# Kernel optimization log

Hardware: AMD Instinct MI355X
Metric: run time of the kernel (lower is better)

## Reference

```python
import jax, jax.numpy as jnp
import numpy as np

TOP_K = 2

def setup_inputs() -> dict:
    key = jax.random.key(0)
    k1, k2 = jax.random.split(key)
    D, E = 4096, 64
    hidden_states = jax.random.normal(k1, (2, 8192, D), dtype=jnp.float32)
    W = jax.random.normal(k2, (E, D), dtype=jnp.float32) / np.sqrt(D)
    b = jnp.zeros((E,), dtype=jnp.float32)
    return {"hidden_states": hidden_states, "W": W, "b": b}

def reference(hidden_states, W, b):
    # gate: logits [B, S, E]
    logits = jnp.einsum('bsd,ed->bse', hidden_states, W) + b
    scores = jax.nn.softmax(logits, axis=-1)
    top_k_values, top_k_indices = jax.lax.top_k(scores, TOP_K)
    return ((top_k_indices, top_k_values), scores)
```

## Files before the change

kernel.cpp:

```cpp
#include <hip/hip_runtime.h>
#include <math.h>

#define D_DIM 4096
#define E_DIM 64
#define TM 32
#define CHK 128
#define NCH (D_DIM / CHK)
#define HC 16384
#define SROW 68
#define WSCALE 1024.0f
#define ISCALE (1.0f / 1024.0f)

typedef __attribute__((ext_vector_type(8))) __fp16 f16x8;
typedef __attribute__((ext_vector_type(2))) __fp16 f16x2;
typedef __attribute__((ext_vector_type(4))) float f32x4;

__device__ inline void split2(const f32x4 a0, const f32x4 a1, f16x8& fh, f16x8& fl) {
    float f[8] = {a0[0], a0[1], a0[2], a0[3], a1[0], a1[1], a1[2], a1[3]};
    union { f16x8 v; f16x2 p[4]; } H, L;
    #pragma unroll
    for (int j = 0; j < 4; ++j) {
        const f16x2 h = __builtin_amdgcn_cvt_pkrtz(f[2*j], f[2*j+1]);
        const float r0 = f[2*j]     - (float)h[0];
        const float r1 = f[2*j + 1] - (float)h[1];
        H.p[j] = h;
        L.p[j] = __builtin_amdgcn_cvt_pkrtz(r0, r1);
    }
    fh = H.v; fl = L.v;
}

__global__ __launch_bounds__(512, 4) void router_fused(
    const float* __restrict__ hs,
    const float* __restrict__ W,
    const float* __restrict__ bias,
    float* __restrict__ out,
    int nTok)
{
    __shared__ __attribute__((aligned(16))) __fp16 wbuf[2][HC];

    const int tid  = threadIdx.x;
    const int lane = tid & 63;
    const int wv   = tid >> 6;
    const int th   = wv >> 2;
    const int eq   = wv & 3;
    const int l15  = lane & 15;
    const int lq   = lane >> 4;
    const int tb   = blockIdx.x * TM;

    const float* aptr = hs + (size_t)(tb + th * 16 + l15) * D_DIM + lq * 8;
    const int erow = (eq * 16 + l15) * 128;
    const int g0   = lq ^ (l15 & 7);

    const int we = tid >> 3;
    const int wa = tid & 7;
    const float* wptr = W + (size_t)we * D_DIM + wa * 16;
    const int wbase = we * 128;
    const int gp0 = ((2 * wa)     ^ (we & 7)) * 8;
    const int gp1 = ((2 * wa + 1) ^ (we & 7)) * 8;

    f32x4 acc = (f32x4){0.f, 0.f, 0.f, 0.f};
    f32x4 ca[8], pa[8], wr[4];

    auto loadA = [&](int ch, f32x4* dst) {
        const float* p = aptr + ch * CHK;
        #pragma unroll
        for (int s = 0; s < 4; ++s) {
            dst[2*s]     = *(const f32x4*)(p + s * 32);
            dst[2*s + 1] = *(const f32x4*)(p + s * 32 + 4);
        }
    };
    auto loadW = [&](int ch) {
        const float* p = wptr + ch * CHK;
        wr[0] = *(const f32x4*)(p);
        wr[1] = *(const f32x4*)(p + 4);
        wr[2] = *(const f32x4*)(p + 8);
        wr[3] = *(const f32x4*)(p + 12);
    };
    auto storeW = [&](int buf) {
        f16x8 h0, l0, h1, l1;
        split2(wr[0] * WSCALE, wr[1] * WSCALE, h0, l0);
        split2(wr[2] * WSCALE, wr[3] * WSCALE, h1, l1);
        __fp16* b = &wbuf[buf][0];
        *(f16x8*)&b[wbase + gp0]        = h0;  *(f16x8*)&b[wbase + gp1]        = h1;
        *(f16x8*)&b[8192 + wbase + gp0] = l0;  *(f16x8*)&b[8192 + wbase + gp1] = l1;
    };
    auto compute = [&](const f32x4* a, int buf) {
        #pragma unroll
        for (int s = 0; s < 4; ++s) {
            f16x8 ah, al;
            split2(a[2*s], a[2*s + 1], ah, al);
            const int go = (g0 ^ (s << 2)) * 8;
            const f16x8 bh = *(const f16x8*)&wbuf[buf][erow + go];
            const f16x8 bl = *(const f16x8*)&wbuf[buf][8192 + erow + go];
            acc = __builtin_amdgcn_mfma_f32_16x16x32_f16(ah, bh, acc, 0, 0, 0);
            acc = __builtin_amdgcn_mfma_f32_16x16x32_f16(ah, bl, acc, 0, 0, 0);
            acc = __builtin_amdgcn_mfma_f32_16x16x32_f16(al, bh, acc, 0, 0, 0);
        }
    };

    loadA(0, ca);
    loadW(0);
    storeW(0);
    __syncthreads();
    int buf = 0;
    #pragma unroll 1
    for (int ch = 0; ch < NCH; ++ch) {
        const bool last = (ch == NCH - 1);
        if (!last) {
            loadA(ch + 1, pa);
            loadW(ch + 1);
        }
        compute(ca, buf);
        if (!last) storeW(buf ^ 1);
        __syncthreads();
        if (!last) {
            #pragma unroll
            for (int i = 0; i < 8; ++i) ca[i] = pa[i];
        }
        buf ^= 1;
    }

    float* sc_lds = (float*)&wbuf[0][0];
    {
        const int e = eq * 16 + l15;
        #pragma unroll
        for (int r = 0; r < 4; ++r)
            sc_lds[(th * 16 + lq * 4 + r) * SROW + e] = acc[r] * ISCALE;
    }
    __syncthreads();

    if (tid < TM * 4) {
        const int token = tid >> 2;
        const int g     = tid & 3;
        const int gtok  = tb + token;

        float* out_idx = out;
        float* out_val = out + (size_t)nTok * 2;
        float* sc      = out + (size_t)nTok * 4;

        const float* srcl = sc_lds + token * SROW + g * 16;
        float v[16];
        #pragma unroll
        for (int j = 0; j < 4; ++j) {
            const f32x4 x = *(const f32x4*)(srcl + j * 4);
            const f32x4 b = *(const f32x4*)(bias + g * 16 + j * 4);
            v[j*4 + 0] = x[0] + b[0];
            v[j*4 + 1] = x[1] + b[1];
            v[j*4 + 2] = x[2] + b[2];
            v[j*4 + 3] = x[3] + b[3];
        }

        float b1 = -INFINITY, b2 = -INFINITY;
        int i1 = 0, i2 = 0;
        #pragma unroll
        for (int j = 0; j < 16; ++j) {
            const float x = v[j];
            const int idx = g * 16 + j;
            if (x > b1)      { b2 = b1; i2 = i1; b1 = x; i1 = idx; }
            else if (x > b2) { b2 = x; i2 = idx; }
        }
        #pragma unroll
        for (int d = 1; d <= 2; d <<= 1) {
            const float ob1 = __shfl_xor(b1, d);
            const int   oi1 = __shfl_xor(i1, d);
            const float ob2 = __shfl_xor(b2, d);
            const int   oi2 = __shfl_xor(i2, d);
            if (ob1 > b1 || (ob1 == b1 && oi1 < i1)) {
                if (b1 > ob2 || (b1 == ob2 && i1 < oi2)) { b2 = b1; i2 = i1; }
                else                                     { b2 = ob2; i2 = oi2; }
                b1 = ob1; i1 = oi1;
            } else {
                if (ob1 > b2 || (ob1 == b2 && oi1 < i2)) { b2 = ob1; i2 = oi1; }
            }
        }
        const float m = b1;

        float e[16];
        float s = 0.f;
        #pragma unroll
        for (int j = 0; j < 16; ++j) { e[j] = __expf(v[j] - m); s += e[j]; }
        s += __shfl_xor(s, 1);
        s += __shfl_xor(s, 2);
        const float inv = 1.f / s;

        if (g == 0) {
            out_idx[(size_t)gtok * 2 + 0] = (float)i1;
            out_idx[(size_t)gtok * 2 + 1] = (float)i2;
            out_val[(size_t)gtok * 2 + 0] = inv;
            out_val[(size_t)gtok * 2 + 1] = __expf(b2 - m) * inv;
        }

        float* dstg = sc + (size_t)gtok * E_DIM + g * 16;
        #pragma unroll
        for (int j = 0; j < 4; ++j) {
            f32x4 o;
            o[0] = e[j*4 + 0] * inv;
            o[1] = e[j*4 + 1] * inv;
            o[2] = e[j*4 + 2] * inv;
            o[3] = e[j*4 + 3] * inv;
            *(f32x4*)(dstg + j * 4) = o;
        }
    }
}

extern "C" void kernel_launch(void* const* d_in, const int* in_sizes, int n_in,
                              void* d_out, int out_size, void* d_ws, size_t ws_size,
                              hipStream_t stream) {
    const float* hs = (const float*)d_in[0];
    const float* W  = (const float*)d_in[1];
    const float* b  = (const float*)d_in[2];
    float* out = (float*)d_out;
    const int nTok = in_sizes[0] / D_DIM;

    router_fused<<<dim3(nTok / TM), dim3(512), 0, stream>>>(hs, W, b, out, nTok);
}
```

Measured before the change: 443.6 us.

## Split-K across waves with W read directly from global, drop LDS weight staging

Each block now handles 16 tokens with 4 waves, each wave covering a quarter of the K dimension for all 64 experts. Partial sums are reduced through LDS before the softmax/top-k. W is loaded straight from global/L2 and split into fp16 hi/lo in registers, so the shared-memory weight double-buffer and the per-chunk __syncthreads go away. In exchange, every block re-reads and re-converts W, which multiplies W traffic and conversion ALU work, and the final reduction is small extra LDS work.

```diff
diff --git a/kernel.cpp b/kernel.cpp
--- a/kernel.cpp
+++ b/kernel.cpp
@@ -3,10 +3,10 @@
 
 #define D_DIM 4096
 #define E_DIM 64
-#define TM 32
-#define CHK 128
-#define NCH (D_DIM / CHK)
-#define HC 16384
+#define TM 16
+#define KQ 1024
+#define CHK 64
+#define NCH (KQ / CHK)
 #define SROW 68
 #define WSCALE 1024.0f
 #define ISCALE (1.0f / 1024.0f)
@@ -29,104 +29,73 @@
     fh = H.v; fl = L.v;
 }
 
-__global__ __launch_bounds__(512, 4) void router_fused(
+__global__ __launch_bounds__(256, 4) void router_fused(
     const float* __restrict__ hs,
     const float* __restrict__ W,
     const float* __restrict__ bias,
     float* __restrict__ out,
     int nTok)
 {
-    __shared__ __attribute__((aligned(16))) __fp16 wbuf[2][HC];
+    __shared__ float sc_lds[4][TM][SROW];
 
     const int tid  = threadIdx.x;
     const int lane = tid & 63;
     const int wv   = tid >> 6;
-    const int th   = wv >> 2;
-    const int eq   = wv & 3;
     const int l15  = lane & 15;
     const int lq   = lane >> 4;
     const int tb   = blockIdx.x * TM;
 
-    const float* aptr = hs + (size_t)(tb + th * 16 + l15) * D_DIM + lq * 8;
-    const int erow = (eq * 16 + l15) * 128;
-    const int g0   = lq ^ (l15 & 7);
+    const float* aptr = hs + (size_t)(tb + l15) * D_DIM + wv * KQ + lq * 8;
+    const float* wptr = W + (size_t)l15 * D_DIM + wv * KQ + lq * 8;
 
-    const int we = tid >> 3;
-    const int wa = tid & 7;
-    const float* wptr = W + (size_t)we * D_DIM + wa * 16;
-    const int wbase = we * 128;
-    const int gp0 = ((2 * wa)     ^ (we & 7)) * 8;
-    const int gp1 = ((2 * wa + 1) ^ (we & 7)) * 8;
+    f32x4 acc[4];
+    #pragma unroll
+    for (int t = 0; t < 4; ++t) acc[t] = (f32x4){0.f, 0.f, 0.f, 0.f};
 
-    f32x4 acc = (f32x4){0.f, 0.f, 0.f, 0.f};
-    f32x4 ca[8], pa[8], wr[4];
+    f32x4 ca[4], pa[4];
 
     auto loadA = [&](int ch, f32x4* dst) {
         const float* p = aptr + ch * CHK;
+        dst[0] = *(const f32x4*)(p);
+        dst[1] = *(const f32x4*)(p + 4);
+        dst[2] = *(const f32x4*)(p + 32);
+        dst[3] = *(const f32x4*)(p + 36);
+    };
+    auto computeChunk = [&](int ch, const f32x4* a) {
         #pragma unroll
-        for (int s = 0; s < 4; ++s) {
-            dst[2*s]     = *(const f32x4*)(p + s * 32);
-            dst[2*s + 1] = *(const f32x4*)(p + s * 32 + 4);
-        }
-    };
-    auto loadW = [&](int ch) {
-        const float* p = wptr + ch * CHK;
-        wr[0] = *(const f32x4*)(p);
-        wr[1] = *(const f32x4*)(p + 4);
-        wr[2] = *(const f32x4*)(p + 8);
-        wr[3] = *(const f32x4*)(p + 12);
-    };
-    auto storeW = [&](int buf) {
-        f16x8 h0, l0, h1, l1;
-        split2(wr[0] * WSCALE, wr[1] * WSCALE, h0, l0);
-        split2(wr[2] * WSCALE, wr[3] * WSCALE, h1, l1);
-        __fp16* b = &wbuf[buf][0];
-        *(f16x8*)&b[wbase + gp0]        = h0;  *(f16x8*)&b[wbase + gp1]        = h1;
-        *(f16x8*)&b[8192 + wbase + gp0] = l0;  *(f16x8*)&b[8192 + wbase + gp1] = l1;
-    };
-    auto compute = [&](const f32x4* a, int buf) {
-        #pragma unroll
-        for (int s = 0; s < 4; ++s) {
+        for (int s = 0; s < 2; ++s) {
             f16x8 ah, al;
             split2(a[2*s], a[2*s + 1], ah, al);
-            const int go = (g0 ^ (s << 2)) * 8;
-            const f16x8 bh = *(const f16x8*)&wbuf[buf][erow + go];
-            const f16x8 bl = *(const f16x8*)&wbuf[buf][8192 + erow + go];
-            acc = __builtin_amdgcn_mfma_f32_16x16x32_f16(ah, bh, acc, 0, 0, 0);
-            acc = __builtin_amdgcn_mfma_f32_16x16x32_f16(ah, bl, acc, 0, 0, 0);
-            acc = __builtin_amdgcn_mfma_f32_16x16x32_f16(al, bh, acc, 0, 0, 0);
+            #pragma unroll
+            for (int t = 0; t < 4; ++t) {
+                const float* p = wptr + (size_t)t * 16 * D_DIM + ch * CHK + s * 32;
+                const f32x4 w0 = *(const f32x4*)(p);
+                const f32x4 w1 = *(const f32x4*)(p + 4);
+                f16x8 bh, bl;
+                split2(w0 * WSCALE, w1 * WSCALE, bh, bl);
+                acc[t] = __builtin_amdgcn_mfma_f32_16x16x32_f16(ah, bh, acc[t], 0, 0, 0);
+                acc[t] = __builtin_amdgcn_mfma_f32_16x16x32_f16(ah, bl, acc[t], 0, 0, 0);
+                acc[t] = __builtin_amdgcn_mfma_f32_16x16x32_f16(al, bh, acc[t], 0, 0, 0);
+            }
         }
     };
 
     loadA(0, ca);
-    loadW(0);
-    storeW(0);
-    __syncthreads();
-    int buf = 0;
     #pragma unroll 1
     for (int ch = 0; ch < NCH; ++ch) {
-        const bool last = (ch == NCH - 1);
-        if (!last) {
-            loadA(ch + 1, pa);
-            loadW(ch + 1);
+        if (ch + 1 < NCH) loadA(ch + 1, pa);
+        computeChunk(ch, ca);
+        if (ch + 1 < NCH) {
+            #pragma unroll
+            for (int i = 0; i < 4; ++i) ca[i] = pa[i];
         }
-        compute(ca, buf);
-        if (!last) storeW(buf ^ 1);
-        __syncthreads();
-        if (!last) {
-            #pragma unroll
-            for (int i = 0; i < 8; ++i) ca[i] = pa[i];
-        }
-        buf ^= 1;
     }
 
-    float* sc_lds = (float*)&wbuf[0][0];
-    {
-        const int e = eq * 16 + l15;
+    #pragma unroll
+    for (int t = 0; t < 4; ++t)
         #pragma unroll
         for (int r = 0; r < 4; ++r)
-            sc_lds[(th * 16 + lq * 4 + r) * SROW + e] = acc[r] * ISCALE;
-    }
+            sc_lds[wv][lq * 4 + r][t * 16 + l15] = acc[t][r] * ISCALE;
     __syncthreads();
 
     if (tid < TM * 4) {
@@ -138,11 +107,15 @@
         float* out_val = out + (size_t)nTok * 2;
         float* sc      = out + (size_t)nTok * 4;
 
-        const float* srcl = sc_lds + token * SROW + g * 16;
         float v[16];
         #pragma unroll
         for (int j = 0; j < 4; ++j) {
-            const f32x4 x = *(const f32x4*)(srcl + j * 4);
+            f32x4 x = *(const f32x4*)&sc_lds[0][token][g * 16 + j * 4];
+            #pragma unroll
+            for (int q = 1; q < 4; ++q) {
+                const f32x4 y = *(const f32x4*)&sc_lds[q][token][g * 16 + j * 4];
+                x[0] += y[0]; x[1] += y[1]; x[2] += y[2]; x[3] += y[3];
+            }
             const f32x4 b = *(const f32x4*)(bias + g * 16 + j * 4);
             v[j*4 + 0] = x[0] + b[0];
             v[j*4 + 1] = x[1] + b[1];
@@ -212,5 +185,5 @@
     float* out = (float*)d_out;
     const int nTok = in_sizes[0] / D_DIM;
 
-    router_fused<<<dim3(nTok / TM), dim3(512), 0, stream>>>(hs, W, b, out, nTok);
+    router_fused<<<dim3(nTok / TM), dim3(256), 0, stream>>>(hs, W, b, out, nTok);
 }
```

Result: no change. 442.4 us (-0.3%).
